# Kernel tuning notes

Measured on AMD Instinct MI355X. Metric: run time of the kernel, lower is better.

Reference implementation:

```python
import jax, jax.numpy as jnp
import numpy as np

N_NODES = 250000
N_EDGES = 8000000
F_IN = 16
N_GRAPHS = 512
BN_EPS = 1e-5


def setup_inputs() -> dict:
    key = jax.random.key(0)
    ks = jax.random.split(key, 16)
    x = jax.random.normal(ks[0], (N_NODES, F_IN), dtype=jnp.float32)
    edge_index = jax.random.randint(ks[1], (2, N_EDGES), 0, N_NODES, dtype=jnp.int64)
    batch = jnp.sort(jax.random.randint(ks[2], (N_NODES,), 0, N_GRAPHS, dtype=jnp.int64))
    def lin(k, fan_in, fan_out):
        s = 1.0 / np.sqrt(fan_in)
        kw, kb = jax.random.split(k)
        W = jax.random.uniform(kw, (fan_in, fan_out), jnp.float32, -s, s)
        b = jax.random.uniform(kb, (fan_out,), jnp.float32, -s, s)
        return W, b
    W1a, b1a = lin(ks[3], F_IN, 32)
    W1b, b1b = lin(ks[4], 32, 16)
    W2a, b2a = lin(ks[5], 16, 16)
    W2b, b2b = lin(ks[6], 16, 16)
    Wfc, bfc = lin(ks[7], 32, 2)
    return {
        'x': x,
        'W1a': W1a, 'b1a': b1a, 'W1b': W1b, 'b1b': b1b,
        'g1': jnp.ones((16,), jnp.float32), 'be1': jnp.zeros((16,), jnp.float32),
        'W2a': W2a, 'b2a': b2a, 'W2b': W2b, 'b2b': b2b,
        'g2': jnp.ones((16,), jnp.float32), 'be2': jnp.zeros((16,), jnp.float32),
        'Wfc': Wfc, 'bfc': bfc,
        'edge_index': edge_index, 'batch': batch,
    }


def _mlp(h, Wa, ba, Wb, bb):
    # Linear -> ReLU -> (Dropout=identity in eval) -> Linear -> ReLU
    h = jax.nn.relu(h @ Wa + ba)
    return jax.nn.relu(h @ Wb + bb)


def _bn(h, gamma, beta):
    # BatchNorm1d over node axis, training-mode batch statistics, biased var
    mean = jnp.mean(h, axis=0)
    var = jnp.mean(jnp.square(h - mean), axis=0)
    return gamma * (h - mean) * jax.lax.rsqrt(var + BN_EPS) + beta


def _gin_conv(h, src, dst, Wa, ba, Wb, bb):
    # GINConv, eps=0: nn((1+eps)*h + sum_{j in N(i)} h_j)
    agg = jax.ops.segment_sum(h[src], dst, num_segments=N_NODES)
    return _mlp(h + agg, Wa, ba, Wb, bb)


def reference(x, W1a, b1a, W1b, b1b, g1, be1, W2a, b2a, W2b, b2b, g2, be2, Wfc, bfc, edge_index, batch):
    src, dst = edge_index[0], edge_index[1]
    h = jax.nn.relu(_bn(_gin_conv(x, src, dst, W1a, b1a, W1b, b1b), g1, be1))
    h = jax.nn.relu(_bn(_gin_conv(h, src, dst, W2a, b2a, W2b, b2b), g2, be2))
    # global max / mean pool over graphs
    x_max = jax.ops.segment_max(h, batch, num_segments=N_GRAPHS)
    x_max = jnp.where(jnp.isfinite(x_max), x_max, 0.0)  # guard empty segments
    counts = jax.ops.segment_sum(jnp.ones((h.shape[0], 1), h.dtype), batch, num_segments=N_GRAPHS)
    x_mean = jax.ops.segment_sum(h, batch, num_segments=N_GRAPHS) / jnp.maximum(counts, 1.0)
    pooled = jnp.concatenate([x_max, x_mean], axis=1)  # [G, 32]
    return pooled @ Wfc + bfc
```

## Files before the change

### kernel.cpp

```cpp
#include <hip/hip_runtime.h>

#define F 16
#define N_GRAPHS_C 512
#define BN_EPS 1e-5f

#define NBSHIFT 8
#define BSZ (1 << NBSHIFT)
#define MAXB 1024
#define SRCBITS 18
#define SRCMASK ((1u << SRCBITS) - 1u)
#define PCHUNK 8192
#define CAP 8960
#define CAPB 9216

__device__ inline unsigned short f2bf(float f) {
    unsigned u = __float_as_uint(f);
    return (unsigned short)((u + 0x7fffu + ((u >> 16) & 1u)) >> 16);
}

__global__ __launch_bounds__(256) void k_scatter(
    const float* __restrict__ h, const int* __restrict__ src,
    const int* __restrict__ dst, float* __restrict__ agg, int n_edges)
{
    int idx = blockIdx.x * 256 + threadIdx.x;
    int tot = n_edges << 2;
    if (idx >= tot) return;
    int e = idx >> 2, q = idx & 3;
    int s = src[e], d = dst[e];
    float4 v = reinterpret_cast<const float4*>(h + (size_t)s * F)[q];
    float* o = agg + (size_t)d * F + q * 4;
    atomicAdd(o + 0, v.x);
    atomicAdd(o + 1, v.y);
    atomicAdd(o + 2, v.z);
    atomicAdd(o + 3, v.w);
}

__global__ __launch_bounds__(256) void k_partition_conv(
    const int* __restrict__ src, const int* __restrict__ dst, int n_edges,
    unsigned* __restrict__ gcur, unsigned* __restrict__ part, int nbk,
    const float* __restrict__ xf, unsigned short* __restrict__ tbf, int n4,
    int npart)
{
    if ((int)blockIdx.x >= npart) {
        int nb = (int)gridDim.x - npart;
        for (int i = ((int)blockIdx.x - npart) * 256 + (int)threadIdx.x;
             i < n4; i += nb * 256) {
            float4 v = reinterpret_cast<const float4*>(xf)[i];
            ushort4 o;
            o.x = f2bf(v.x); o.y = f2bf(v.y); o.z = f2bf(v.z); o.w = f2bf(v.w);
            reinterpret_cast<ushort4*>(tbf)[i] = o;
        }
        return;
    }

    __shared__ unsigned hist[MAXB];
    __shared__ unsigned offs[MAXB + 1];
    __shared__ unsigned lcur[MAXB];
    __shared__ unsigned gbase[MAXB];
    __shared__ unsigned stage[PCHUNK];
    __shared__ unsigned wsum[4];

    const int t = threadIdx.x;
    const int lane = t & 63, w = t >> 6;

    int base = blockIdx.x * PCHUNK;
    int cnt = n_edges - base; if (cnt > PCHUNK) cnt = PCHUNK;
    if (cnt <= 0) return;

    for (int i = t; i < nbk; i += 256) hist[i] = 0;
    __syncthreads();
    for (int i = t; i < cnt; i += 256)
        atomicAdd(&hist[dst[base + i] >> NBSHIFT], 1u);
    __syncthreads();
    int t4 = t * 4;
    unsigned h0 = (t4 + 0 < nbk) ? hist[t4 + 0] : 0u;
    unsigned h1 = (t4 + 1 < nbk) ? hist[t4 + 1] : 0u;
    unsigned h2 = (t4 + 2 < nbk) ? hist[t4 + 2] : 0u;
    unsigned h3 = (t4 + 3 < nbk) ? hist[t4 + 3] : 0u;
    unsigned tsum = h0 + h1 + h2 + h3;
    unsigned incl = tsum;
#pragma unroll
    for (int d = 1; d < 64; d <<= 1) {
        unsigned u = __shfl_up(incl, d);
        if (lane >= d) incl += u;
    }
    if (lane == 63) wsum[w] = incl;
    __syncthreads();
    unsigned wo = 0;
    for (int ww = 0; ww < w; ww++) wo += wsum[ww];
    unsigned ex = wo + incl - tsum;
    if (t4 + 0 < nbk) offs[t4 + 0] = ex;
    if (t4 + 1 < nbk) offs[t4 + 1] = ex + h0;
    if (t4 + 2 < nbk) offs[t4 + 2] = ex + h0 + h1;
    if (t4 + 3 < nbk) offs[t4 + 3] = ex + h0 + h1 + h2;
    if (t == 0) offs[nbk] = (unsigned)cnt;
    __syncthreads();
    for (int b = t; b < nbk; b += 256) {
        lcur[b] = offs[b];
        unsigned hb = hist[b];
        gbase[b] = hb ? ((unsigned)b * CAPB + atomicAdd(&gcur[b], hb)) : 0u;
    }
    __syncthreads();
    for (int i = t; i < cnt; i += 256) {
        int d = dst[base + i];
        int b = d >> NBSHIFT;
        unsigned p = (unsigned)src[base + i] | (((unsigned)d & (BSZ - 1u)) << SRCBITS);
        stage[atomicAdd(&lcur[b], 1u)] = p;
    }
    __syncthreads();
    for (int i = t; i < cnt; i += 256) {
        int lo = 0, hi = nbk;
        while (hi - lo > 1) { int m = (lo + hi) >> 1; if (offs[m] <= (unsigned)i) lo = m; else hi = m; }
        part[gbase[lo] + ((unsigned)i - offs[lo])] = stage[i];
    }
}

__global__ __launch_bounds__(256, 4) void k_aggregate(
    const unsigned short* __restrict__ hb, const unsigned* __restrict__ part,
    const unsigned* __restrict__ gcur, float* __restrict__ agg, int n_nodes)
{
    __shared__ unsigned stage[CAP];
    __shared__ unsigned hist[BSZ];
    __shared__ unsigned offs[BSZ];
    __shared__ unsigned cursor[BSZ];
    __shared__ unsigned wsum[4];

    const int b = blockIdx.x;
    const unsigned s = (unsigned)b * CAPB;
    const unsigned e = s + gcur[b];
    const int t = threadIdx.x;
    const int lane = t & 63, w = t >> 6;

    float acc[F];
#pragma unroll
    for (int k = 0; k < F; k++) acc[k] = 0.f;

#define ACC8(U, B0) \
    acc[B0+0] += __uint_as_float((U).x << 16); \
    acc[B0+1] += __uint_as_float((U).x & 0xffff0000u); \
    acc[B0+2] += __uint_as_float((U).y << 16); \
    acc[B0+3] += __uint_as_float((U).y & 0xffff0000u); \
    acc[B0+4] += __uint_as_float((U).z << 16); \
    acc[B0+5] += __uint_as_float((U).z & 0xffff0000u); \
    acc[B0+6] += __uint_as_float((U).w << 16); \
    acc[B0+7] += __uint_as_float((U).w & 0xffff0000u);

    for (unsigned base = s; base < e; base += CAP) {
        unsigned cnt = e - base; if (cnt > CAP) cnt = CAP;

        hist[t] = 0;
        __syncthreads();
        for (unsigned i = t; i < cnt; i += 256)
            atomicAdd(&hist[part[base + i] >> SRCBITS], 1u);
        __syncthreads();
        unsigned hv = hist[t];
        unsigned inc = hv;
#pragma unroll
        for (int d = 1; d < 64; d <<= 1) {
            unsigned up = __shfl_up(inc, d);
            if (lane >= d) inc += up;
        }
        if (lane == 63) wsum[w] = inc;
        __syncthreads();
        unsigned wo = 0;
        for (int ww = 0; ww < w; ww++) wo += wsum[ww];
        unsigned excl = wo + inc - hv;
        offs[t] = excl;
        cursor[t] = excl;
        __syncthreads();
        for (unsigned i = t; i < cnt; i += 256) {
            unsigned p = part[base + i];
            unsigned pos = atomicAdd(&cursor[p >> SRCBITS], 1u);
            stage[pos] = p & SRCMASK;
        }
        __syncthreads();
        unsigned k = offs[t];
        const unsigned kend = cursor[t];
        while (k + 4 <= kend) {
            unsigned s0 = stage[k + 0], s1 = stage[k + 1];
            unsigned s2 = stage[k + 2], s3 = stage[k + 3];
            const uint4* p0 = reinterpret_cast<const uint4*>(hb + (size_t)s0 * F);
            const uint4* p1 = reinterpret_cast<const uint4*>(hb + (size_t)s1 * F);
            const uint4* p2 = reinterpret_cast<const uint4*>(hb + (size_t)s2 * F);
            const uint4* p3 = reinterpret_cast<const uint4*>(hb + (size_t)s3 * F);
            uint4 a0 = p0[0], b0 = p0[1];
            uint4 a1 = p1[0], b1 = p1[1];
            uint4 a2 = p2[0], b2 = p2[1];
            uint4 a3 = p3[0], b3 = p3[1];
            ACC8(a0, 0) ACC8(b0, 8)
            ACC8(a1, 0) ACC8(b1, 8)
            ACC8(a2, 0) ACC8(b2, 8)
            ACC8(a3, 0) ACC8(b3, 8)
            k += 4;
        }
        for (; k < kend; ++k) {
            unsigned s0 = stage[k];
            const uint4* p0 = reinterpret_cast<const uint4*>(hb + (size_t)s0 * F);
            uint4 a0 = p0[0], b0 = p0[1];
            ACC8(a0, 0) ACC8(b0, 8)
        }
        __syncthreads();
    }
#undef ACC8

    int r = (b << NBSHIFT) + t;
    if (r < n_nodes) {
        float4* op = reinterpret_cast<float4*>(agg + (size_t)r * F);
        op[0] = make_float4(acc[0],  acc[1],  acc[2],  acc[3]);
        op[1] = make_float4(acc[4],  acc[5],  acc[6],  acc[7]);
        op[2] = make_float4(acc[8],  acc[9],  acc[10], acc[11]);
        op[3] = make_float4(acc[12], acc[13], acc[14], acc[15]);
    }
}

template <int HID, bool BF>
__global__ __launch_bounds__(256) void k_mlp_stats(
    const void* __restrict__ xin, const float* agg,
    const float* __restrict__ Wa, const float* __restrict__ ba,
    const float* __restrict__ Wb, const float* __restrict__ bb,
    float* hpre, float* __restrict__ stats, int n_nodes)
{
    __shared__ float sWa[F * HID], sba[HID], sWb[HID * F], sbb[F];
    for (int i = threadIdx.x; i < F * HID; i += 256) sWa[i] = Wa[i];
    for (int i = threadIdx.x; i < HID * F; i += 256) sWb[i] = Wb[i];
    if (threadIdx.x < HID) sba[threadIdx.x] = ba[threadIdx.x];
    if (threadIdx.x < F)   sbb[threadIdx.x] = bb[threadIdx.x];
    __syncthreads();

    int node = blockIdx.x * 256 + threadIdx.x;
    float o[F];
    if (node < n_nodes) {
        float v[F];
        if (BF) {
            const uint4* xp = reinterpret_cast<const uint4*>(
                (const unsigned short*)xin + (size_t)node * F);
            uint4 u0 = xp[0], u1 = xp[1];
            v[0]  = __uint_as_float(u0.x << 16); v[1]  = __uint_as_float(u0.x & 0xffff0000u);
            v[2]  = __uint_as_float(u0.y << 16); v[3]  = __uint_as_float(u0.y & 0xffff0000u);
            v[4]  = __uint_as_float(u0.z << 16); v[5]  = __uint_as_float(u0.z & 0xffff0000u);
            v[6]  = __uint_as_float(u0.w << 16); v[7]  = __uint_as_float(u0.w & 0xffff0000u);
            v[8]  = __uint_as_float(u1.x << 16); v[9]  = __uint_as_float(u1.x & 0xffff0000u);
            v[10] = __uint_as_float(u1.y << 16); v[11] = __uint_as_float(u1.y & 0xffff0000u);
            v[12] = __uint_as_float(u1.z << 16); v[13] = __uint_as_float(u1.z & 0xffff0000u);
            v[14] = __uint_as_float(u1.w << 16); v[15] = __uint_as_float(u1.w & 0xffff0000u);
        } else {
            const float4* xp = reinterpret_cast<const float4*>(
                (const float*)xin + (size_t)node * F);
#pragma unroll
            for (int q = 0; q < 4; q++) {
                float4 a = xp[q];
                v[q * 4 + 0] = a.x; v[q * 4 + 1] = a.y;
                v[q * 4 + 2] = a.z; v[q * 4 + 3] = a.w;
            }
        }
        const float4* ap = reinterpret_cast<const float4*>(agg + (size_t)node * F);
#pragma unroll
        for (int q = 0; q < 4; q++) {
            float4 bq = ap[q];
            v[q * 4 + 0] += bq.x; v[q * 4 + 1] += bq.y;
            v[q * 4 + 2] += bq.z; v[q * 4 + 3] += bq.w;
        }
        float hid[HID];
#pragma unroll
        for (int j = 0; j < HID; j++) hid[j] = sba[j];
#pragma unroll
        for (int k = 0; k < F; k++) {
            float vk = v[k];
#pragma unroll
            for (int j = 0; j < HID; j++) hid[j] = fmaf(vk, sWa[k * HID + j], hid[j]);
        }
#pragma unroll
        for (int j = 0; j < HID; j++) hid[j] = fmaxf(hid[j], 0.f);
#pragma unroll
        for (int j = 0; j < F; j++) o[j] = sbb[j];
#pragma unroll
        for (int k = 0; k < HID; k++) {
            float hk = hid[k];
#pragma unroll
            for (int j = 0; j < F; j++) o[j] = fmaf(hk, sWb[k * F + j], o[j]);
        }
#pragma unroll
        for (int j = 0; j < F; j++) o[j] = fmaxf(o[j], 0.f);
        float4* op = reinterpret_cast<float4*>(hpre + (size_t)node * F);
        op[0] = make_float4(o[0], o[1], o[2], o[3]);
        op[1] = make_float4(o[4], o[5], o[6], o[7]);
        op[2] = make_float4(o[8], o[9], o[10], o[11]);
        op[3] = make_float4(o[12], o[13], o[14], o[15]);
    } else {
#pragma unroll
        for (int j = 0; j < F; j++) o[j] = 0.f;
    }

    __shared__ float red[4][2 * F];
    int lane = threadIdx.x & 63, wid = threadIdx.x >> 6;
#pragma unroll
    for (int j = 0; j < F; j++) {
        float s = o[j], ss = o[j] * o[j];
#pragma unroll
        for (int off = 32; off; off >>= 1) {
            s  += __shfl_down(s, off);
            ss += __shfl_down(ss, off);
        }
        if (lane == 0) { red[wid][j] = s; red[wid][F + j] = ss; }
    }
    __syncthreads();
    if (threadIdx.x < 2 * F) {
        float t = red[0][threadIdx.x] + red[1][threadIdx.x] +
                  red[2][threadIdx.x] + red[3][threadIdx.x];
        atomicAdd(&stats[threadIdx.x], t);
    }
}

template <bool BFOUT>
__global__ __launch_bounds__(256) void k_bn_relu(
    const float* __restrict__ hpre, const float* __restrict__ stats,
    const float* __restrict__ gamma, const float* __restrict__ beta,
    void* __restrict__ hout, int n_nodes)
{
    int idx = blockIdx.x * 256 + threadIdx.x;
    int tot = n_nodes * 4;
    if (idx >= tot) return;
    int q = idx & 3;
    float4 v = reinterpret_cast<const float4*>(hpre)[idx];
    float invN = 1.f / (float)n_nodes;
    float r[4];
    float vin[4] = {v.x, v.y, v.z, v.w};
#pragma unroll
    for (int t = 0; t < 4; t++) {
        int j = q * 4 + t;
        float mean = stats[j] * invN;
        float var  = stats[F + j] * invN - mean * mean;
        float sc   = gamma[j] * rsqrtf(var + BN_EPS);
        r[t] = fmaxf((vin[t] - mean) * sc + beta[j], 0.f);
    }
    if (BFOUT) {
        ushort4 o;
        o.x = f2bf(r[0]); o.y = f2bf(r[1]); o.z = f2bf(r[2]); o.w = f2bf(r[3]);
        reinterpret_cast<ushort4*>(hout)[idx] = o;
    } else {
        reinterpret_cast<float4*>(hout)[idx] = make_float4(r[0], r[1], r[2], r[3]);
    }
}

template <bool BFIN>
__global__ __launch_bounds__(256) void k_pool_fc(
    const void* __restrict__ h, const int* __restrict__ batch,
    const float* __restrict__ Wfc, const float* __restrict__ bfc,
    float* __restrict__ out, int n_nodes)
{
    int g = blockIdx.x;
    int lo = 0, hi = n_nodes;
    while (lo < hi) { int m = (lo + hi) >> 1; if (batch[m] < g) lo = m + 1; else hi = m; }
    int start = lo;
    hi = n_nodes;
    while (lo < hi) { int m = (lo + hi) >> 1; if (batch[m] < g + 1) lo = m + 1; else hi = m; }
    int end = lo;

    float mx[F], sm[F];
#pragma unroll
    for (int j = 0; j < F; j++) { mx[j] = 0.f; sm[j] = 0.f; }

    for (int i = start + (int)threadIdx.x; i < end; i += 256) {
        float v[F];
        if (BFIN) {
            const uint4* p = reinterpret_cast<const uint4*>(
                (const unsigned short*)h + (size_t)i * F);
            uint4 u0 = p[0], u1 = p[1];
            v[0]  = __uint_as_float(u0.x << 16); v[1]  = __uint_as_float(u0.x & 0xffff0000u);
            v[2]  = __uint_as_float(u0.y << 16); v[3]  = __uint_as_float(u0.y & 0xffff0000u);
            v[4]  = __uint_as_float(u0.z << 16); v[5]  = __uint_as_float(u0.z & 0xffff0000u);
            v[6]  = __uint_as_float(u0.w << 16); v[7]  = __uint_as_float(u0.w & 0xffff0000u);
            v[8]  = __uint_as_float(u1.x << 16); v[9]  = __uint_as_float(u1.x & 0xffff0000u);
            v[10] = __uint_as_float(u1.y << 16); v[11] = __uint_as_float(u1.y & 0xffff0000u);
            v[12] = __uint_as_float(u1.z << 16); v[13] = __uint_as_float(u1.z & 0xffff0000u);
            v[14] = __uint_as_float(u1.w << 16); v[15] = __uint_as_float(u1.w & 0xffff0000u);
        } else {
            const float4* p = reinterpret_cast<const float4*>(
                (const float*)h + (size_t)i * F);
#pragma unroll
            for (int q = 0; q < 4; q++) {
                float4 vv = p[q];
                v[q * 4 + 0] = vv.x; v[q * 4 + 1] = vv.y;
                v[q * 4 + 2] = vv.z; v[q * 4 + 3] = vv.w;
            }
        }
#pragma unroll
        for (int j = 0; j < F; j++) { mx[j] = fmaxf(mx[j], v[j]); sm[j] += v[j]; }
    }
#pragma unroll
    for (int j = 0; j < F; j++) {
#pragma unroll
        for (int off = 32; off; off >>= 1) {
            mx[j] = fmaxf(mx[j], __shfl_down(mx[j], off));
            sm[j] += __shfl_down(sm[j], off);
        }
    }
    __shared__ float rmx[4][F], rsm[4][F];
    int lane = threadIdx.x & 63, wid = threadIdx.x >> 6;
    if (lane == 0) {
#pragma unroll
        for (int j = 0; j < F; j++) { rmx[wid][j] = mx[j]; rsm[wid][j] = sm[j]; }
    }
    __syncthreads();
    if (threadIdx.x == 0) {
        float pooled[2 * F];
        int cnt = end - start;
        float inv = 1.f / (float)(cnt > 0 ? cnt : 1);
#pragma unroll
        for (int j = 0; j < F; j++) {
            float m = fmaxf(fmaxf(rmx[0][j], rmx[1][j]), fmaxf(rmx[2][j], rmx[3][j]));
            float s = rsm[0][j] + rsm[1][j] + rsm[2][j] + rsm[3][j];
            pooled[j]     = m;
            pooled[F + j] = s * inv;
        }
#pragma unroll
        for (int c = 0; c < 2; c++) {
            float acc = bfc[c];
#pragma unroll
            for (int k = 0; k < 2 * F; k++) acc = fmaf(pooled[k], Wfc[k * 2 + c], acc);
            out[g * 2 + c] = acc;
        }
    }
}

extern "C" void kernel_launch(void* const* d_in, const int* in_sizes, int n_in,
                              void* d_out, int out_size, void* d_ws, size_t ws_size,
                              hipStream_t stream) {
    const float* x    = (const float*)d_in[0];
    const float* W1a  = (const float*)d_in[1];
    const float* b1a  = (const float*)d_in[2];
    const float* W1b  = (const float*)d_in[3];
    const float* b1b  = (const float*)d_in[4];
    const float* g1   = (const float*)d_in[5];
    const float* be1  = (const float*)d_in[6];
    const float* W2a  = (const float*)d_in[7];
    const float* b2a  = (const float*)d_in[8];
    const float* W2b  = (const float*)d_in[9];
    const float* b2b  = (const float*)d_in[10];
    const float* g2   = (const float*)d_in[11];
    const float* be2  = (const float*)d_in[12];
    const float* Wfc  = (const float*)d_in[13];
    const float* bfc  = (const float*)d_in[14];
    const int*   eidx = (const int*)d_in[15];
    const int*   batch= (const int*)d_in[16];

    const int n_nodes = in_sizes[0] / F;
    const int n_edges = in_sizes[15] / 2;
    const int* src = eidx;
    const int* dst = eidx + n_edges;

    const size_t NBf = (size_t)n_nodes * F * sizeof(float);
    const size_t NBh = (size_t)n_nodes * F * sizeof(unsigned short);
    const int nbk = (n_nodes + BSZ - 1) >> NBSHIFT;
    float* out = (float*)d_out;

    const int nblk_nodes = (n_nodes + 255) / 256;
    const int nblk_el4   = (n_nodes * 4 + 255) / 256;

    size_t off = 0;
    auto take = [&](size_t bytes) { size_t o = off; off = (off + bytes + 255) & ~(size_t)255; return o; };
    size_t meta_bytes = (size_t)(nbk + 64) * sizeof(unsigned);
    size_t meta_off = take(meta_bytes);
    size_t part_off = take((size_t)nbk * CAPB * sizeof(unsigned));
    size_t agg_off  = take(NBf);
    size_t tbf_off  = take(NBh);
    bool fast = (nbk <= MAXB) && (n_nodes <= (1 << SRCBITS)) && (off <= ws_size);

    char* ws = (char*)d_ws;
    if (fast) {
        unsigned* meta    = (unsigned*)(ws + meta_off);
        unsigned* gcur    = meta;
        float*    stats1  = (float*)(meta + nbk);
        float*    stats2  = stats1 + 32;
        unsigned* part    = (unsigned*)(ws + part_off);
        float*    agg     = (float*)(ws + agg_off);
        unsigned short* tbf = (unsigned short*)(ws + tbf_off);

        hipMemsetAsync(meta, 0, meta_bytes, stream);
        int npart = (n_edges + PCHUNK - 1) / PCHUNK;
        int nconv = nbk;
        k_partition_conv<<<npart + nconv, 256, 0, stream>>>(
            src, dst, n_edges, gcur, part, nbk, x, tbf, n_nodes * 4, npart);

        k_aggregate<<<nbk, 256, 0, stream>>>(tbf, part, gcur, agg, n_nodes);
        k_mlp_stats<32, false><<<nblk_nodes, 256, 0, stream>>>(x, agg, W1a, b1a, W1b, b1b,
                                                               agg , stats1, n_nodes);
        k_bn_relu<true><<<nblk_el4, 256, 0, stream>>>(agg, stats1, g1, be1, tbf, n_nodes);

        k_aggregate<<<nbk, 256, 0, stream>>>(tbf, part, gcur, agg, n_nodes);
        k_mlp_stats<16, true><<<nblk_nodes, 256, 0, stream>>>(tbf, agg, W2a, b2a, W2b, b2b,
                                                              agg , stats2, n_nodes);
        k_bn_relu<true><<<nblk_el4, 256, 0, stream>>>(agg, stats2, g2, be2, tbf, n_nodes);

        k_pool_fc<true><<<N_GRAPHS_C, 256, 0, stream>>>(tbf, batch, Wfc, bfc, out, n_nodes);
    } else {
        float* hpre = (float*)(ws);
        float* hbuf = (float*)(ws + NBf);
        float* agg  = (float*)(ws + 2 * NBf);
        float* stats= (float*)(ws + 3 * NBf);
        const int nblk_edges = (int)(((long long)n_edges * 4 + 255) / 256);

        hipMemsetAsync(agg, 0, NBf, stream);
        hipMemsetAsync(stats, 0, 2 * F * sizeof(float), stream);
        k_scatter<<<nblk_edges, 256, 0, stream>>>(x, src, dst, agg, n_edges);
        k_mlp_stats<32, false><<<nblk_nodes, 256, 0, stream>>>(x, agg, W1a, b1a, W1b, b1b,
                                                               hpre, stats, n_nodes);
        k_bn_relu<false><<<nblk_el4, 256, 0, stream>>>(hpre, stats, g1, be1, hbuf, n_nodes);

        hipMemsetAsync(agg, 0, NBf, stream);
        hipMemsetAsync(stats, 0, 2 * F * sizeof(float), stream);
        k_scatter<<<nblk_edges, 256, 0, stream>>>(hbuf, src, dst, agg, n_edges);
        k_mlp_stats<16, false><<<nblk_nodes, 256, 0, stream>>>(hbuf, agg, W2a, b2a, W2b, b2b,
                                                               hpre, stats, n_nodes);
        k_bn_relu<false><<<nblk_el4, 256, 0, stream>>>(hpre, stats, g2, be2, hbuf, n_nodes);

        k_pool_fc<false><<<N_GRAPHS_C, 256, 0, stream>>>(hbuf, batch, Wfc, bfc, out, n_nodes);
    }
}
```

Baseline: 533.8 us.

## Sort edge buckets once and reuse across both aggregations; fuse final BN into pooling

The per-bucket counting sort of edges by destination row moves into a separate k_rowsort kernel that runs once and writes the sorted sources plus per-row offsets back to global memory. Both aggregation passes then read the presorted lists directly, with no shared-memory histogram or staging step, which removes the sort work that was repeated in each layer. The second BN+ReLU pass is folded into the pooling kernel, which now applies the scale and shift to the fp32 pre-activations, so one elementwise kernel and its bf16 write are gone. The cost is an extra kernel launch, an in-place write of the edge partition, and pooling reading fp32 data instead of bf16.

```diff
diff --git a/kernel.cpp b/kernel.cpp
--- a/kernel.cpp
+++ b/kernel.cpp
@@ -10,7 +10,6 @@
 #define SRCBITS 18
 #define SRCMASK ((1u << SRCBITS) - 1u)
 #define PCHUNK 8192
-#define CAP 8960
 #define CAPB 9216
 
 __device__ inline unsigned short f2bf(float f) {
@@ -115,11 +114,11 @@
     }
 }
 
-__global__ __launch_bounds__(256, 4) void k_aggregate(
-    const unsigned short* __restrict__ hb, const unsigned* __restrict__ part,
-    const unsigned* __restrict__ gcur, float* __restrict__ agg, int n_nodes)
-{
-    __shared__ unsigned stage[CAP];
+__global__ __launch_bounds__(256, 4) void k_rowsort(
+    unsigned* __restrict__ part, const unsigned* __restrict__ gcur,
+    unsigned* __restrict__ offs2)
+{
+    __shared__ unsigned stage[CAPB];
     __shared__ unsigned hist[BSZ];
     __shared__ unsigned offs[BSZ];
     __shared__ unsigned cursor[BSZ];
@@ -127,13 +126,56 @@
 
     const int b = blockIdx.x;
     const unsigned s = (unsigned)b * CAPB;
-    const unsigned e = s + gcur[b];
+    const unsigned n = gcur[b];
     const int t = threadIdx.x;
     const int lane = t & 63, w = t >> 6;
 
+    hist[t] = 0;
+    __syncthreads();
+    for (unsigned i = t; i < n; i += 256)
+        atomicAdd(&hist[part[s + i] >> SRCBITS], 1u);
+    __syncthreads();
+    unsigned hv = hist[t];
+    unsigned inc = hv;
+#pragma unroll
+    for (int d = 1; d < 64; d <<= 1) {
+        unsigned up = __shfl_up(inc, d);
+        if (lane >= d) inc += up;
+    }
+    if (lane == 63) wsum[w] = inc;
+    __syncthreads();
+    unsigned wo = 0;
+    for (int ww = 0; ww < w; ww++) wo += wsum[ww];
+    unsigned excl = wo + inc - hv;
+    offs[t] = excl;
+    cursor[t] = excl;
+    offs2[(size_t)b * BSZ + t] = excl;
+    __syncthreads();
+    for (unsigned i = t; i < n; i += 256) {
+        unsigned p = part[s + i];
+        unsigned pos = atomicAdd(&cursor[p >> SRCBITS], 1u);
+        stage[pos] = p & SRCMASK;
+    }
+    __syncthreads();
+    for (unsigned i = t; i < n; i += 256)
+        part[s + i] = stage[i];
+}
+
+__global__ __launch_bounds__(256) void k_aggregate(
+    const unsigned short* __restrict__ hb, const unsigned* __restrict__ part,
+    const unsigned* __restrict__ gcur, const unsigned* __restrict__ offs2,
+    float* __restrict__ agg, int n_nodes)
+{
+    const int b = blockIdx.x;
+    const unsigned s = (unsigned)b * CAPB;
+    const int t = threadIdx.x;
+
+    unsigned k    = offs2[(size_t)b * BSZ + t];
+    unsigned kend = (t < BSZ - 1) ? offs2[(size_t)b * BSZ + t + 1] : gcur[b];
+
     float acc[F];
 #pragma unroll
-    for (int k = 0; k < F; k++) acc[k] = 0.f;
+    for (int q = 0; q < F; q++) acc[q] = 0.f;
 
 #define ACC8(U, B0) \
     acc[B0+0] += __uint_as_float((U).x << 16); \
@@ -145,61 +187,28 @@
     acc[B0+6] += __uint_as_float((U).w << 16); \
     acc[B0+7] += __uint_as_float((U).w & 0xffff0000u);
 
-    for (unsigned base = s; base < e; base += CAP) {
-        unsigned cnt = e - base; if (cnt > CAP) cnt = CAP;
-
-        hist[t] = 0;
-        __syncthreads();
-        for (unsigned i = t; i < cnt; i += 256)
-            atomicAdd(&hist[part[base + i] >> SRCBITS], 1u);
-        __syncthreads();
-        unsigned hv = hist[t];
-        unsigned inc = hv;
-#pragma unroll
-        for (int d = 1; d < 64; d <<= 1) {
-            unsigned up = __shfl_up(inc, d);
-            if (lane >= d) inc += up;
-        }
-        if (lane == 63) wsum[w] = inc;
-        __syncthreads();
-        unsigned wo = 0;
-        for (int ww = 0; ww < w; ww++) wo += wsum[ww];
-        unsigned excl = wo + inc - hv;
-        offs[t] = excl;
-        cursor[t] = excl;
-        __syncthreads();
-        for (unsigned i = t; i < cnt; i += 256) {
-            unsigned p = part[base + i];
-            unsigned pos = atomicAdd(&cursor[p >> SRCBITS], 1u);
-            stage[pos] = p & SRCMASK;
-        }
-        __syncthreads();
-        unsigned k = offs[t];
-        const unsigned kend = cursor[t];
-        while (k + 4 <= kend) {
-            unsigned s0 = stage[k + 0], s1 = stage[k + 1];
-            unsigned s2 = stage[k + 2], s3 = stage[k + 3];
-            const uint4* p0 = reinterpret_cast<const uint4*>(hb + (size_t)s0 * F);
-            const uint4* p1 = reinterpret_cast<const uint4*>(hb + (size_t)s1 * F);
-            const uint4* p2 = reinterpret_cast<const uint4*>(hb + (size_t)s2 * F);
-            const uint4* p3 = reinterpret_cast<const uint4*>(hb + (size_t)s3 * F);
-            uint4 a0 = p0[0], b0 = p0[1];
-            uint4 a1 = p1[0], b1 = p1[1];
-            uint4 a2 = p2[0], b2 = p2[1];
-            uint4 a3 = p3[0], b3 = p3[1];
-            ACC8(a0, 0) ACC8(b0, 8)
-            ACC8(a1, 0) ACC8(b1, 8)
-            ACC8(a2, 0) ACC8(b2, 8)
-            ACC8(a3, 0) ACC8(b3, 8)
-            k += 4;
-        }
-        for (; k < kend; ++k) {
-            unsigned s0 = stage[k];
-            const uint4* p0 = reinterpret_cast<const uint4*>(hb + (size_t)s0 * F);
-            uint4 a0 = p0[0], b0 = p0[1];
-            ACC8(a0, 0) ACC8(b0, 8)
-        }
-        __syncthreads();
+    while (k + 4 <= kend) {
+        unsigned s0 = part[s + k + 0], s1 = part[s + k + 1];
+        unsigned s2 = part[s + k + 2], s3 = part[s + k + 3];
+        const uint4* p0 = reinterpret_cast<const uint4*>(hb + (size_t)s0 * F);
+        const uint4* p1 = reinterpret_cast<const uint4*>(hb + (size_t)s1 * F);
+        const uint4* p2 = reinterpret_cast<const uint4*>(hb + (size_t)s2 * F);
+        const uint4* p3 = reinterpret_cast<const uint4*>(hb + (size_t)s3 * F);
+        uint4 a0 = p0[0], b0 = p0[1];
+        uint4 a1 = p1[0], b1 = p1[1];
+        uint4 a2 = p2[0], b2 = p2[1];
+        uint4 a3 = p3[0], b3 = p3[1];
+        ACC8(a0, 0) ACC8(b0, 8)
+        ACC8(a1, 0) ACC8(b1, 8)
+        ACC8(a2, 0) ACC8(b2, 8)
+        ACC8(a3, 0) ACC8(b3, 8)
+        k += 4;
+    }
+    for (; k < kend; ++k) {
+        unsigned s0 = part[s + k];
+        const uint4* p0 = reinterpret_cast<const uint4*>(hb + (size_t)s0 * F);
+        uint4 a0 = p0[0], b0 = p0[1];
+        ACC8(a0, 0) ACC8(b0, 8)
     }
 #undef ACC8
 
@@ -311,11 +320,10 @@
     }
 }
 
-template <bool BFOUT>
-__global__ __launch_bounds__(256) void k_bn_relu(
+__global__ __launch_bounds__(256) void k_bn_relu_bf(
     const float* __restrict__ hpre, const float* __restrict__ stats,
     const float* __restrict__ gamma, const float* __restrict__ beta,
-    void* __restrict__ hout, int n_nodes)
+    unsigned short* __restrict__ hout, int n_nodes)
 {
     int idx = blockIdx.x * 256 + threadIdx.x;
     int tot = n_nodes * 4;
@@ -333,18 +341,40 @@
         float sc   = gamma[j] * rsqrtf(var + BN_EPS);
         r[t] = fmaxf((vin[t] - mean) * sc + beta[j], 0.f);
     }
-    if (BFOUT) {
-        ushort4 o;
-        o.x = f2bf(r[0]); o.y = f2bf(r[1]); o.z = f2bf(r[2]); o.w = f2bf(r[3]);
-        reinterpret_cast<ushort4*>(hout)[idx] = o;
-    } else {
-        reinterpret_cast<float4*>(hout)[idx] = make_float4(r[0], r[1], r[2], r[3]);
-    }
-}
-
-template <bool BFIN>
-__global__ __launch_bounds__(256) void k_pool_fc(
-    const void* __restrict__ h, const int* __restrict__ batch,
+    ushort4 o;
+    o.x = f2bf(r[0]); o.y = f2bf(r[1]); o.z = f2bf(r[2]); o.w = f2bf(r[3]);
+    reinterpret_cast<ushort4*>(hout)[idx] = o;
+}
+
+__global__ __launch_bounds__(256) void k_bn_relu_f32(
+    const float* __restrict__ hpre, const float* __restrict__ stats,
+    const float* __restrict__ gamma, const float* __restrict__ beta,
+    float* __restrict__ hout, int n_nodes)
+{
+    int idx = blockIdx.x * 256 + threadIdx.x;
+    int tot = n_nodes * 4;
+    if (idx >= tot) return;
+    int q = idx & 3;
+    float4 v = reinterpret_cast<const float4*>(hpre)[idx];
+    float invN = 1.f / (float)n_nodes;
+    float r[4];
+    float vin[4] = {v.x, v.y, v.z, v.w};
+#pragma unroll
+    for (int t = 0; t < 4; t++) {
+        int j = q * 4 + t;
+        float mean = stats[j] * invN;
+        float var  = stats[F + j] * invN - mean * mean;
+        float sc   = gamma[j] * rsqrtf(var + BN_EPS);
+        r[t] = fmaxf((vin[t] - mean) * sc + beta[j], 0.f);
+    }
+    reinterpret_cast<float4*>(hout)[idx] = make_float4(r[0], r[1], r[2], r[3]);
+}
+
+template <bool APPLYBN>
+__global__ __launch_bounds__(256) void k_pool_bn_fc(
+    const float* __restrict__ hpre, const float* __restrict__ stats,
+    const float* __restrict__ gamma, const float* __restrict__ beta,
+    const int* __restrict__ batch,
     const float* __restrict__ Wfc, const float* __restrict__ bfc,
     float* __restrict__ out, int n_nodes)
 {
@@ -356,36 +386,40 @@
     while (lo < hi) { int m = (lo + hi) >> 1; if (batch[m] < g + 1) lo = m + 1; else hi = m; }
     int end = lo;
 
+    float scl[F], sh[F];
+    if (APPLYBN) {
+        float invN = 1.f / (float)n_nodes;
+#pragma unroll
+        for (int j = 0; j < F; j++) {
+            float mean = stats[j] * invN;
+            float var  = stats[F + j] * invN - mean * mean;
+            float sc   = gamma[j] * rsqrtf(var + BN_EPS);
+            scl[j] = sc;
+            sh[j]  = beta[j] - mean * sc;
+        }
+    } else {
+#pragma unroll
+        for (int j = 0; j < F; j++) { scl[j] = 1.f; sh[j] = 0.f; }
+    }
+
     float mx[F], sm[F];
 #pragma unroll
     for (int j = 0; j < F; j++) { mx[j] = 0.f; sm[j] = 0.f; }
 
     for (int i = start + (int)threadIdx.x; i < end; i += 256) {
-        float v[F];
-        if (BFIN) {
-            const uint4* p = reinterpret_cast<const uint4*>(
-                (const unsigned short*)h + (size_t)i * F);
-            uint4 u0 = p[0], u1 = p[1];
-            v[0]  = __uint_as_float(u0.x << 16); v[1]  = __uint_as_float(u0.x & 0xffff0000u);
-            v[2]  = __uint_as_float(u0.y << 16); v[3]  = __uint_as_float(u0.y & 0xffff0000u);
-            v[4]  = __uint_as_float(u0.z << 16); v[5]  = __uint_as_float(u0.z & 0xffff0000u);
-            v[6]  = __uint_as_float(u0.w << 16); v[7]  = __uint_as_float(u0.w & 0xffff0000u);
-            v[8]  = __uint_as_float(u1.x << 16); v[9]  = __uint_as_float(u1.x & 0xffff0000u);
-            v[10] = __uint_as_float(u1.y << 16); v[11] = __uint_as_float(u1.y & 0xffff0000u);
-            v[12] = __uint_as_float(u1.z << 16); v[13] = __uint_as_float(u1.z & 0xffff0000u);
-            v[14] = __uint_as_float(u1.w << 16); v[15] = __uint_as_float(u1.w & 0xffff0000u);
-        } else {
-            const float4* p = reinterpret_cast<const float4*>(
-                (const float*)h + (size_t)i * F);
-#pragma unroll
-            for (int q = 0; q < 4; q++) {
-                float4 vv = p[q];
-                v[q * 4 + 0] = vv.x; v[q * 4 + 1] = vv.y;
-                v[q * 4 + 2] = vv.z; v[q * 4 + 3] = vv.w;
-            }
-        }
-#pragma unroll
-        for (int j = 0; j < F; j++) { mx[j] = fmaxf(mx[j], v[j]); sm[j] += v[j]; }
+        const float4* p = reinterpret_cast<const float4*>(hpre + (size_t)i * F);
+#pragma unroll
+        for (int q = 0; q < 4; q++) {
+            float4 vv = p[q];
+            float v0 = fmaxf(fmaf(vv.x, scl[q*4+0], sh[q*4+0]), 0.f);
+            float v1 = fmaxf(fmaf(vv.y, scl[q*4+1], sh[q*4+1]), 0.f);
+            float v2 = fmaxf(fmaf(vv.z, scl[q*4+2], sh[q*4+2]), 0.f);
+            float v3 = fmaxf(fmaf(vv.w, scl[q*4+3], sh[q*4+3]), 0.f);
+            mx[q*4+0] = fmaxf(mx[q*4+0], v0); sm[q*4+0] += v0;
+            mx[q*4+1] = fmaxf(mx[q*4+1], v1); sm[q*4+1] += v1;
+            mx[q*4+2] = fmaxf(mx[q*4+2], v2); sm[q*4+2] += v2;
+            mx[q*4+3] = fmaxf(mx[q*4+3], v3); sm[q*4+3] += v3;
+        }
     }
 #pragma unroll
     for (int j = 0; j < F; j++) {
@@ -460,10 +494,11 @@
     size_t off = 0;
     auto take = [&](size_t bytes) { size_t o = off; off = (off + bytes + 255) & ~(size_t)255; return o; };
     size_t meta_bytes = (size_t)(nbk + 64) * sizeof(unsigned);
-    size_t meta_off = take(meta_bytes);
-    size_t part_off = take((size_t)nbk * CAPB * sizeof(unsigned));
-    size_t agg_off  = take(NBf);
-    size_t tbf_off  = take(NBh);
+    size_t meta_off  = take(meta_bytes);
+    size_t offs2_off = take((size_t)nbk * BSZ * sizeof(unsigned));
+    size_t part_off  = take((size_t)nbk * CAPB * sizeof(unsigned));
+    size_t agg_off   = take(NBf);
+    size_t tbf_off   = take(NBh);
     bool fast = (nbk <= MAXB) && (n_nodes <= (1 << SRCBITS)) && (off <= ws_size);
 
     char* ws = (char*)d_ws;
@@ -472,6 +507,7 @@
         unsigned* gcur    = meta;
         float*    stats1  = (float*)(meta + nbk);
         float*    stats2  = stats1 + 32;
+        unsigned* offs2   = (unsigned*)(ws + offs2_off);
         unsigned* part    = (unsigned*)(ws + part_off);
         float*    agg     = (float*)(ws + agg_off);
         unsigned short* tbf = (unsigned short*)(ws + tbf_off);
@@ -481,18 +517,19 @@
         int nconv = nbk;
         k_partition_conv<<<npart + nconv, 256, 0, stream>>>(
             src, dst, n_edges, gcur, part, nbk, x, tbf, n_nodes * 4, npart);
-
-        k_aggregate<<<nbk, 256, 0, stream>>>(tbf, part, gcur, agg, n_nodes);
+        k_rowsort<<<nbk, 256, 0, stream>>>(part, gcur, offs2);
+
+        k_aggregate<<<nbk, 256, 0, stream>>>(tbf, part, gcur, offs2, agg, n_nodes);
         k_mlp_stats<32, false><<<nblk_nodes, 256, 0, stream>>>(x, agg, W1a, b1a, W1b, b1b,
                                                                agg , stats1, n_nodes);
-        k_bn_relu<true><<<nblk_el4, 256, 0, stream>>>(agg, stats1, g1, be1, tbf, n_nodes);
-
-        k_aggregate<<<nbk, 256, 0, stream>>>(tbf, part, gcur, agg, n_nodes);
+        k_bn_relu_bf<<<nblk_el4, 256, 0, stream>>>(agg, stats1, g1, be1, tbf, n_nodes);
+
+        k_aggregate<<<nbk, 256, 0, stream>>>(tbf, part, gcur, offs2, agg, n_nodes);
         k_mlp_stats<16, true><<<nblk_nodes, 256, 0, stream>>>(tbf, agg, W2a, b2a, W2b, b2b,
                                                               agg , stats2, n_nodes);
-        k_bn_relu<true><<<nblk_el4, 256, 0, stream>>>(agg, stats2, g2, be2, tbf, n_nodes);
-
-        k_pool_fc<true><<<N_GRAPHS_C, 256, 0, stream>>>(tbf, batch, Wfc, bfc, out, n_nodes);
+
+        k_pool_bn_fc<true><<<N_GRAPHS_C, 256, 0, stream>>>(agg, stats2, g2, be2,
+                                                           batch, Wfc, bfc, out, n_nodes);
     } else {
         float* hpre = (float*)(ws);
         float* hbuf = (float*)(ws + NBf);
@@ -505,15 +542,16 @@
         k_scatter<<<nblk_edges, 256, 0, stream>>>(x, src, dst, agg, n_edges);
         k_mlp_stats<32, false><<<nblk_nodes, 256, 0, stream>>>(x, agg, W1a, b1a, W1b, b1b,
                                                                hpre, stats, n_nodes);
-        k_bn_relu<false><<<nblk_el4, 256, 0, stream>>>(hpre, stats, g1, be1, hbuf, n_nodes);
+        k_bn_relu_f32<<<nblk_el4, 256, 0, stream>>>(hpre, stats, g1, be1, hbuf, n_nodes);
 
         hipMemsetAsync(agg, 0, NBf, stream);
         hipMemsetAsync(stats, 0, 2 * F * sizeof(float), stream);
         k_scatter<<<nblk_edges, 256, 0, stream>>>(hbuf, src, dst, agg, n_edges);
         k_mlp_stats<16, false><<<nblk_nodes, 256, 0, stream>>>(hbuf, agg, W2a, b2a, W2b, b2b,
                                                                hpre, stats, n_nodes);
-        k_bn_relu<false><<<nblk_el4, 256, 0, stream>>>(hpre, stats, g2, be2, hbuf, n_nodes);
-
-        k_pool_fc<false><<<N_GRAPHS_C, 256, 0, stream>>>(hbuf, batch, Wfc, bfc, out, n_nodes);
-    }
-}
+        k_bn_relu_f32<<<nblk_el4, 256, 0, stream>>>(hpre, stats, g2, be2, hbuf, n_nodes);
+
+        k_pool_bn_fc<false><<<N_GRAPHS_C, 256, 0, stream>>>(hbuf, nullptr, nullptr, nullptr,
+                                                            batch, Wfc, bfc, out, n_nodes);
+    }
+}
```

After: 613.0 us. 14.8% more time.
